# Optimization experiments

Measured on AMD Instinct MI355X. Metric: run time of the kernel, lower is better.

Reference implementation:

```python
import jax, jax.numpy as jnp
import numpy as np

K = 16  # top-k patches kept (module default)

def setup_inputs() -> dict:
    key = jax.random.key(0)
    ks = jax.random.split(key, 5)
    N, D, A, H = 100000, 1024, 128, 256
    x = jax.random.normal(ks[0], (N, D), dtype=jnp.float32)
    Wa1 = jax.random.normal(ks[1], (D, A), dtype=jnp.float32) * (1.0 / np.sqrt(D))
    ba1 = jnp.zeros((A,), dtype=jnp.float32)
    Wa2 = jax.random.normal(ks[2], (A, 1), dtype=jnp.float32) * (1.0 / np.sqrt(A))
    ba2 = jnp.zeros((1,), dtype=jnp.float32)
    Wc1 = jax.random.normal(ks[3], (D, H), dtype=jnp.float32) * (1.0 / np.sqrt(D))
    bc1 = jnp.zeros((H,), dtype=jnp.float32)
    Wc2 = jax.random.normal(ks[4], (H, 1), dtype=jnp.float32) * (1.0 / np.sqrt(H))
    bc2 = jnp.zeros((1,), dtype=jnp.float32)
    return {"x": x, "Wa1": Wa1, "ba1": ba1, "Wa2": Wa2, "ba2": ba2,
            "Wc1": Wc1, "bc1": bc1, "Wc2": Wc2, "bc2": bc2}

def reference(x, Wa1, ba1, Wa2, ba2, Wc1, bc1, Wc2, bc2):
    # attention logits: Linear -> tanh -> Linear, shape [N]
    scores = (jnp.tanh(x @ Wa1 + ba1) @ Wa2 + ba2)[:, 0]
    # top-k selection over patch dim (k < N here)
    top_vals, top_idx = jax.lax.top_k(scores, K)       # [K], [K]
    x_k = x[top_idx]                                    # [K, D] gather
    attn_w = jax.nn.softmax(top_vals)                   # renormalise over k
    slide_embedding = attn_w @ x_k                      # [D] weighted sum
    # classifier MLP (dropout is identity in eval)
    h = jax.nn.relu(slide_embedding @ Wc1 + bc1)
    logit = (h @ Wc2 + bc2)[0]
    # scatter attention weights back into full-length vector
    full_weights = jnp.zeros(x.shape[0], dtype=x.dtype).at[top_idx].set(attn_w)
    return logit, slide_embedding, full_weights, top_idx
```

## Files before the change

### kernel.cpp

```cpp
#include <hip/hip_runtime.h>
#include <cstddef>
#include <cstdint>

#define N_PATCH 100000
#define D_IN    1024
#define A_DIM   128
#define H_DIM   256
#define KTOP    16

#define OUT_LOGIT 0
#define OUT_EMB   1
#define OUT_FW    (1 + D_IN)
#define OUT_TOPI  (OUT_FW + N_PATCH)

#define WS_SCORES 0
#define WS_CANDV  (N_PATCH)
#define WS_CANDI  (N_PATCH + 4096)
#define WS_EMB    (N_PATCH + 2 * 4096)
#define WS_HPART  (WS_EMB + D_IN)
#define WS_WPK    (WS_HPART + 16 * H_DIM)

#define NB2A  256
#define CHUNK 391

typedef __attribute__((ext_vector_type(8))) short bf8_t;
typedef __attribute__((ext_vector_type(4))) float f4_t;

__global__ __launch_bounds__(256) void k_prepack(
    const float* __restrict__ Wa1, uint4* __restrict__ wpk)
{
    int t = blockIdx.x * 256 + threadIdx.x;
    int lane = t & 63;
    int part = (t >> 6) & 1;
    int nt   = (t >> 7) & 7;
    int ks   = t >> 10;
    int n  = nt * 16 + (lane & 15);
    int k0 = ks * 32 + ((lane >> 4) * 8);
    union { ushort u[8]; uint4 v; } o;
    #pragma unroll
    for (int j = 0; j < 8; ++j) {
        float w = Wa1[(size_t)(k0 + j) * A_DIM + n];
        uint b = __float_as_uint(w);
        if (part == 0) {
            o.u[j] = (ushort)(b >> 16);
        } else {
            float hf = __uint_as_float(b & 0xffff0000u);
            o.u[j] = (ushort)(__float_as_uint(w - hf) >> 16);
        }
    }
    wpk[t] = o.v;
}

__device__ __forceinline__ void split8(const float4& a, const float4& b,
                                       bf8_t& hi, bf8_t& lo)
{
    union { float f[8]; uint u[8]; float4 v4[2]; } X;
    X.v4[0] = a; X.v4[1] = b;
    union { uint u[4]; bf8_t v; } H, L;
    #pragma unroll
    for (int j = 0; j < 4; ++j) {
        uint x0 = X.u[2 * j], x1 = X.u[2 * j + 1];
        H.u[j] = __builtin_amdgcn_perm(x1, x0, 0x07060302);
        float l0 = X.f[2 * j]     - __uint_as_float(x0 & 0xffff0000u);
        float l1 = X.f[2 * j + 1] - __uint_as_float(x1 & 0xffff0000u);
        L.u[j] = __builtin_amdgcn_perm(__float_as_uint(l1), __float_as_uint(l0), 0x07060302);
    }
    hi = H.v; lo = L.v;
}

#define MFMA_BF16 __builtin_amdgcn_mfma_f32_16x16x32_bf16

#define BAR_LDS() do {                                          \
    asm volatile("s_waitcnt lgkmcnt(0)" ::: "memory");          \
    __builtin_amdgcn_s_barrier();                               \
    asm volatile("" ::: "memory");                              \
} while (0)

#define SCORE_STEP(KS, CUR) do {                                               \
    bf8_t ahi0, alo0, ahi1, alo1;                                              \
    split8(A##CUR[0], A##CUR[1], ahi0, alo0);                                  \
    split8(A##CUR[2], A##CUR[3], ahi1, alo1);                                  \
    if ((KS) < 31) {                                                           \
        _Pragma("unroll")                                                      \
        for (int i = 0; i < 4; ++i) sB[(CUR) ^ 1][tid + i * 256] = bpre[i];    \
    }                                                                          \
    {                                                                          \
        const int kact = (s0 + (KS) + 2) & 31;    \
        _Pragma("unroll")                                                      \
        for (int i = 0; i < 4; ++i) bpre[i] = wpk[kact * 1024 + tid + i * 256];\
        A##CUR[0] = *(const float4*)(pa0 + kact * 32);                         \
        A##CUR[1] = *(const float4*)(pa0 + kact * 32 + 4);                     \
        A##CUR[2] = *(const float4*)(pa1 + kact * 32);                         \
        A##CUR[3] = *(const float4*)(pa1 + kact * 32 + 4);                     \
    }                                                                          \
    const bf8_t* sBf = (const bf8_t*)sB[CUR];                                  \
    _Pragma("unroll")                                                          \
    for (int nt = 0; nt < 8; nt += 2) {                                        \
        bf8_t bh0 = sBf[(nt * 2 + 0) * 64 + ln];                               \
        bf8_t bl0 = sBf[(nt * 2 + 1) * 64 + ln];                               \
        bf8_t bh1 = sBf[(nt * 2 + 2) * 64 + ln];                               \
        bf8_t bl1 = sBf[(nt * 2 + 3) * 64 + ln];                               \
        acc[0][nt]     = MFMA_BF16(ahi0, bh0, acc[0][nt],     0, 0, 0);        \
        acc[1][nt]     = MFMA_BF16(ahi1, bh0, acc[1][nt],     0, 0, 0);        \
        acc[0][nt + 1] = MFMA_BF16(ahi0, bh1, acc[0][nt + 1], 0, 0, 0);        \
        acc[1][nt + 1] = MFMA_BF16(ahi1, bh1, acc[1][nt + 1], 0, 0, 0);        \
        acc[0][nt]     = MFMA_BF16(alo0, bh0, acc[0][nt],     0, 0, 0);        \
        acc[1][nt]     = MFMA_BF16(alo1, bh0, acc[1][nt],     0, 0, 0);        \
        acc[0][nt + 1] = MFMA_BF16(alo0, bh1, acc[0][nt + 1], 0, 0, 0);        \
        acc[1][nt + 1] = MFMA_BF16(alo1, bh1, acc[1][nt + 1], 0, 0, 0);        \
        acc[0][nt]     = MFMA_BF16(ahi0, bl0, acc[0][nt],     0, 0, 0);        \
        acc[1][nt]     = MFMA_BF16(ahi1, bl0, acc[1][nt],     0, 0, 0);        \
        acc[0][nt + 1] = MFMA_BF16(ahi0, bl1, acc[0][nt + 1], 0, 0, 0);        \
        acc[1][nt + 1] = MFMA_BF16(ahi1, bl1, acc[1][nt + 1], 0, 0, 0);        \
    }                                                                          \
    BAR_LDS();                                                                 \
} while (0)

__global__ __launch_bounds__(256) void k_scores(
    const float* __restrict__ x, const uint4* __restrict__ wpk,
    const float* __restrict__ ba1, const float* __restrict__ Wa2,
    const float* __restrict__ ba2, float* __restrict__ scores)
{
    __shared__ uint4 sB[2][1024];

    const int tid = threadIdx.x;
    const int ln  = tid & 63;
    const int q   = ln >> 4;
    const int c   = ln & 15;
    const int wv  = tid >> 6;
    const int row0 = blockIdx.x * 128 + wv * 32;
    const int s0   = blockIdx.x & 31;

    const int r0 = min(row0 + c,      N_PATCH - 1);
    const int r1 = min(row0 + 16 + c, N_PATCH - 1);
    const float* pa0 = x + (size_t)r0 * D_IN + q * 8;
    const float* pa1 = x + (size_t)r1 * D_IN + q * 8;

    f4_t acc[2][8];
    #pragma unroll
    for (int rt = 0; rt < 2; ++rt)
        #pragma unroll
        for (int nt = 0; nt < 8; ++nt)
            acc[rt][nt] = (f4_t){0.f, 0.f, 0.f, 0.f};

    uint4 bpre[4];
    {
        uint4 b0[4];
        #pragma unroll
        for (int i = 0; i < 4; ++i) b0[i] = wpk[s0 * 1024 + tid + i * 256];
        #pragma unroll
        for (int i = 0; i < 4; ++i) sB[0][tid + i * 256] = b0[i];
    }
    {
        const int k1 = (s0 + 1) & 31;
        #pragma unroll
        for (int i = 0; i < 4; ++i) bpre[i] = wpk[k1 * 1024 + tid + i * 256];
    }

    float4 A0[4], A1[4];
    {
        const int ka = s0;
        const int kb = (s0 + 1) & 31;
        A0[0] = *(const float4*)(pa0 + ka * 32);
        A0[1] = *(const float4*)(pa0 + ka * 32 + 4);
        A0[2] = *(const float4*)(pa1 + ka * 32);
        A0[3] = *(const float4*)(pa1 + ka * 32 + 4);
        A1[0] = *(const float4*)(pa0 + kb * 32);
        A1[1] = *(const float4*)(pa0 + kb * 32 + 4);
        A1[2] = *(const float4*)(pa1 + kb * 32);
        A1[3] = *(const float4*)(pa1 + kb * 32 + 4);
    }

    BAR_LDS();

    for (int ks = 0; ks < 32; ks += 2) {
        SCORE_STEP(ks,     0);
        SCORE_STEP(ks + 1, 1);
    }

    float b1v[8], w2v[8];
    #pragma unroll
    for (int nt = 0; nt < 8; ++nt) {
        b1v[nt] = ba1[nt * 16 + c];
        w2v[nt] = Wa2[nt * 16 + c];
    }
    const float b2 = ba2[0];

    #pragma unroll
    for (int rt = 0; rt < 2; ++rt)
        #pragma unroll
        for (int reg = 0; reg < 4; ++reg) {
            float p = 0.f;
            #pragma unroll
            for (int nt = 0; nt < 8; ++nt)
                p += tanhf(acc[rt][nt][reg] + b1v[nt]) * w2v[nt];
            #pragma unroll
            for (int off = 1; off < 16; off <<= 1)
                p += __shfl_xor(p, off, 64);
            if (c == 0) {
                int row = row0 + rt * 16 + q * 4 + reg;
                if (row < N_PATCH) scores[row] = p + b2;
            }
        }
}

__global__ __launch_bounds__(256) void k_topk_local(
    const float* __restrict__ scores, float* __restrict__ candv,
    int* __restrict__ candi, float* __restrict__ out_fw)
{
    __shared__ float sv[512];
    __shared__ float rv[256];
    __shared__ int   rs[256];
    const int tid  = threadIdx.x;
    const int base = blockIdx.x * CHUNK;

    for (int i = tid; i < 512; i += 256) {
        int g = base + i;
        sv[i] = (i < CHUNK && g < N_PATCH) ? scores[g] : -1e30f;
    }
    for (int i = tid; i < CHUNK; i += 256) {
        int g = base + i;
        if (g < N_PATCH) out_fw[g] = 0.f;
    }
    __syncthreads();

    for (int r = 0; r < KTOP; ++r) {
        float v1 = sv[tid], v2 = sv[tid + 256];
        float bv; int bs;
        if (v2 > v1) { bv = v2; bs = tid + 256; } else { bv = v1; bs = tid; }
        rv[tid] = bv; rs[tid] = bs;
        __syncthreads();
        for (int off = 128; off > 0; off >>= 1) {
            if (tid < off) {
                float ov = rv[tid + off]; int os = rs[tid + off];
                if (ov > rv[tid] || (ov == rv[tid] && os < rs[tid])) {
                    rv[tid] = ov; rs[tid] = os;
                }
            }
            __syncthreads();
        }
        if (tid == 0) {
            int s = rs[0];
            candv[blockIdx.x * KTOP + r] = rv[0];
            candi[blockIdx.x * KTOP + r] = base + s;
            sv[s] = -1e30f;
        }
        __syncthreads();
    }
}

__global__ __launch_bounds__(256) void k_finalize(
    const float* __restrict__ candv, const int* __restrict__ candi,
    const float* __restrict__ x, float* __restrict__ out,
    float* __restrict__ emb)
{
    __shared__ float cv[4096];
    __shared__ int   ci[4096];
    __shared__ float rv[256];
    __shared__ int   rgx[256];
    __shared__ int   rsl[256];
    __shared__ float topv[KTOP];
    __shared__ int   topi[KTOP];
    __shared__ float attn[KTOP];
    const int tid = threadIdx.x;

    for (int i = tid; i < 4096; i += 256) { cv[i] = candv[i]; ci[i] = candi[i]; }
    __syncthreads();

    for (int r = 0; r < KTOP; ++r) {
        float bv = -1e38f; int bg = 0x7fffffff; int bs = tid * 16;
        #pragma unroll
        for (int i = 0; i < 16; ++i) {
            int s = tid * 16 + i;
            float v = cv[s]; int g = ci[s];
            if (v > bv || (v == bv && g < bg)) { bv = v; bg = g; bs = s; }
        }
        rv[tid] = bv; rgx[tid] = bg; rsl[tid] = bs;
        __syncthreads();
        for (int off = 128; off > 0; off >>= 1) {
            if (tid < off) {
                if (rv[tid + off] > rv[tid] ||
                    (rv[tid + off] == rv[tid] && rgx[tid + off] < rgx[tid])) {
                    rv[tid] = rv[tid + off]; rgx[tid] = rgx[tid + off]; rsl[tid] = rsl[tid + off];
                }
            }
            __syncthreads();
        }
        if (tid == 0) {
            topv[r] = rv[0]; topi[r] = rgx[0]; cv[rsl[0]] = -1e30f;
        }
        __syncthreads();
    }

    if (tid == 0) {
        float mx = topv[0];
        float s = 0.f;
        for (int k2 = 0; k2 < KTOP; ++k2) {
            float e = expf(topv[k2] - mx);
            attn[k2] = e; s += e;
        }
        float inv = 1.f / s;
        for (int k2 = 0; k2 < KTOP; ++k2) attn[k2] *= inv;
    }
    __syncthreads();

    if (tid < KTOP) {
        out[OUT_TOPI + tid] = (float)topi[tid];
        out[OUT_FW + topi[tid]] = attn[tid];
    }

    float4 e = {0.f, 0.f, 0.f, 0.f};
    #pragma unroll
    for (int k2 = 0; k2 < KTOP; ++k2) {
        const float a = attn[k2];
        const float4 xv = *(const float4*)(x + (size_t)topi[k2] * D_IN + tid * 4);
        e.x = fmaf(a, xv.x, e.x);
        e.y = fmaf(a, xv.y, e.y);
        e.z = fmaf(a, xv.z, e.z);
        e.w = fmaf(a, xv.w, e.w);
    }
    out[OUT_EMB + tid * 4 + 0] = e.x;
    out[OUT_EMB + tid * 4 + 1] = e.y;
    out[OUT_EMB + tid * 4 + 2] = e.z;
    out[OUT_EMB + tid * 4 + 3] = e.w;
    *(float4*)(emb + tid * 4) = e;
}

__global__ __launch_bounds__(256) void k_mlp1(
    const float* __restrict__ emb, const float* __restrict__ Wc1,
    float* __restrict__ hpart)
{
    __shared__ float se[64];
    const int b = blockIdx.x, tid = threadIdx.x;
    if (tid < 64) se[tid] = emb[b * 64 + tid];
    __syncthreads();
    float p = 0.f;
    #pragma unroll 8
    for (int d = 0; d < 64; ++d)
        p = fmaf(se[d], Wc1[(size_t)(b * 64 + d) * H_DIM + tid], p);
    hpart[b * H_DIM + tid] = p;
}

__global__ __launch_bounds__(256) void k_logit(
    const float* __restrict__ hpart, const float* __restrict__ bc1,
    const float* __restrict__ Wc2, const float* __restrict__ bc2,
    float* __restrict__ out)
{
    __shared__ float red[256];
    const int tid = threadIdx.x;
    float h = bc1[tid];
    #pragma unroll
    for (int i = 0; i < 16; ++i) h += hpart[i * H_DIM + tid];
    h = fmaxf(h, 0.f) * Wc2[tid];
    red[tid] = h;
    __syncthreads();
    for (int off = 128; off > 0; off >>= 1) {
        if (tid < off) red[tid] += red[tid + off];
        __syncthreads();
    }
    if (tid == 0) out[OUT_LOGIT] = red[0] + bc2[0];
}

extern "C" void kernel_launch(void* const* d_in, const int* in_sizes, int n_in,
                              void* d_out, int out_size, void* d_ws, size_t ws_size,
                              hipStream_t stream)
{
    const float* x   = (const float*)d_in[0];
    const float* Wa1 = (const float*)d_in[1];
    const float* ba1 = (const float*)d_in[2];
    const float* Wa2 = (const float*)d_in[3];
    const float* ba2 = (const float*)d_in[4];
    const float* Wc1 = (const float*)d_in[5];
    const float* bc1 = (const float*)d_in[6];
    const float* Wc2 = (const float*)d_in[7];
    const float* bc2 = (const float*)d_in[8];
    float* out = (float*)d_out;
    float* ws  = (float*)d_ws;

    float* scores = ws + WS_SCORES;
    float* candv  = ws + WS_CANDV;
    int*   candi  = (int*)(ws + WS_CANDI);
    float* emb    = ws + WS_EMB;
    float* hpart  = ws + WS_HPART;
    uint4* wpk    = (uint4*)(ws + WS_WPK);

    dim3 blk(256);
    k_prepack<<<128, blk, 0, stream>>>(Wa1, wpk);
    k_scores<<<(N_PATCH + 127) / 128, blk, 0, stream>>>(x, wpk, ba1, Wa2, ba2, scores);
    k_topk_local<<<NB2A, blk, 0, stream>>>(scores, candv, candi, out + OUT_FW);
    k_finalize<<<1, blk, 0, stream>>>(candv, candi, x, out, emb);
    k_mlp1<<<16, blk, 0, stream>>>(emb, Wc1, hpart);
    k_logit<<<1, blk, 0, stream>>>(hpart, bc1, Wc2, bc2, out);
}
```

Measured before the change: 718.3 us.

## Score in single bf16 MFMA pass, then rescore top candidates exactly in fp32

The score GEMM drops the hi/lo bf16 split (three MFMAs per tile) and uses a single round-to-nearest bf16 product. Weight prepacking halves and the A conversion uses the hardware packed bf16 convert. To keep the selection and softmax accurate, the finalize kernel recomputes exact fp32 scores for the 16 selected rows, re-sorts them and builds attention from those values. The risk is that bf16 error changes which rows enter the top-16 candidate set. The single-block fp32 rescore also adds serial work to finalize.

Result: slower. 830.0 us (+15.5%).

```diff
diff --git a/kernel.cpp b/kernel.cpp
--- a/kernel.cpp
+++ b/kernel.cpp
@@ -31,41 +31,27 @@
 {
     int t = blockIdx.x * 256 + threadIdx.x;
     int lane = t & 63;
-    int part = (t >> 6) & 1;
-    int nt   = (t >> 7) & 7;
-    int ks   = t >> 10;
+    int nt   = (t >> 6) & 7;
+    int ks   = t >> 9;
     int n  = nt * 16 + (lane & 15);
     int k0 = ks * 32 + ((lane >> 4) * 8);
     union { ushort u[8]; uint4 v; } o;
     #pragma unroll
     for (int j = 0; j < 8; ++j) {
-        float w = Wa1[(size_t)(k0 + j) * A_DIM + n];
-        uint b = __float_as_uint(w);
-        if (part == 0) {
-            o.u[j] = (ushort)(b >> 16);
-        } else {
-            float hf = __uint_as_float(b & 0xffff0000u);
-            o.u[j] = (ushort)(__float_as_uint(w - hf) >> 16);
-        }
+        uint b = __float_as_uint(Wa1[(size_t)(k0 + j) * A_DIM + n]);
+        o.u[j] = (ushort)((b + 0x7fffu + ((b >> 16) & 1u)) >> 16);
     }
     wpk[t] = o.v;
 }
 
-__device__ __forceinline__ void split8(const float4& a, const float4& b,
-                                       bf8_t& hi, bf8_t& lo)
-{
-    union { float f[8]; uint u[8]; float4 v4[2]; } X;
-    X.v4[0] = a; X.v4[1] = b;
-    union { uint u[4]; bf8_t v; } H, L;
-    #pragma unroll
-    for (int j = 0; j < 4; ++j) {
-        uint x0 = X.u[2 * j], x1 = X.u[2 * j + 1];
-        H.u[j] = __builtin_amdgcn_perm(x1, x0, 0x07060302);
-        float l0 = X.f[2 * j]     - __uint_as_float(x0 & 0xffff0000u);
-        float l1 = X.f[2 * j + 1] - __uint_as_float(x1 & 0xffff0000u);
-        L.u[j] = __builtin_amdgcn_perm(__float_as_uint(l1), __float_as_uint(l0), 0x07060302);
-    }
-    hi = H.v; lo = L.v;
+__device__ __forceinline__ void cvt8(const float4& a, const float4& b, bf8_t& out)
+{
+    union { uint u[4]; bf8_t v; } O;
+    asm("v_cvt_pk_bf16_f32 %0, %1, %2" : "=v"(O.u[0]) : "v"(a.x), "v"(a.y));
+    asm("v_cvt_pk_bf16_f32 %0, %1, %2" : "=v"(O.u[1]) : "v"(a.z), "v"(a.w));
+    asm("v_cvt_pk_bf16_f32 %0, %1, %2" : "=v"(O.u[2]) : "v"(b.x), "v"(b.y));
+    asm("v_cvt_pk_bf16_f32 %0, %1, %2" : "=v"(O.u[3]) : "v"(b.z), "v"(b.w));
+    out = O.v;
 }
 
 #define MFMA_BF16 __builtin_amdgcn_mfma_f32_16x16x32_bf16
@@ -76,44 +62,35 @@
     asm volatile("" ::: "memory");                              \
 } while (0)
 
-#define SCORE_STEP(KS, CUR) do {                                               \
-    bf8_t ahi0, alo0, ahi1, alo1;                                              \
-    split8(A##CUR[0], A##CUR[1], ahi0, alo0);                                  \
-    split8(A##CUR[2], A##CUR[3], ahi1, alo1);                                  \
-    if ((KS) < 31) {                                                           \
+#define SCORE_STEP(IT, PAR, CUR) do {                                          \
+    bf8_t ah0, ah1;                                                            \
+    cvt8(A##CUR[0], A##CUR[1], ah0);                                           \
+    cvt8(A##CUR[2], A##CUR[3], ah1);                                           \
+    if ((PAR) == 0) {                                                          \
         _Pragma("unroll")                                                      \
-        for (int i = 0; i < 4; ++i) sB[(CUR) ^ 1][tid + i * 256] = bpre[i];    \
+        for (int i = 0; i < 4; ++i) sB[bufp ^ 1][tid + i * 256] = bpre[i];     \
+        const int vtp = (t0 + (IT) + 2) & 15;                                  \
+        _Pragma("unroll")                                                      \
+        for (int i = 0; i < 4; ++i) bpre[i] = wpk[vtp * 1024 + tid + i * 256]; \
     }                                                                          \
     {                                                                          \
-        const int kact = (s0 + (KS) + 2) & 31;    \
-        _Pragma("unroll")                                                      \
-        for (int i = 0; i < 4; ++i) bpre[i] = wpk[kact * 1024 + tid + i * 256];\
-        A##CUR[0] = *(const float4*)(pa0 + kact * 32);                         \
-        A##CUR[1] = *(const float4*)(pa0 + kact * 32 + 4);                     \
-        A##CUR[2] = *(const float4*)(pa1 + kact * 32);                         \
-        A##CUR[3] = *(const float4*)(pa1 + kact * 32 + 4);                     \
+        const int kg2 = (((t0 + (IT) + 1) & 15) * 2 + (PAR)) * 32;             \
+        A##CUR[0] = *(const float4*)(pa0 + kg2);                               \
+        A##CUR[1] = *(const float4*)(pa0 + kg2 + 4);                           \
+        A##CUR[2] = *(const float4*)(pa1 + kg2);                               \
+        A##CUR[3] = *(const float4*)(pa1 + kg2 + 4);                           \
     }                                                                          \
-    const bf8_t* sBf = (const bf8_t*)sB[CUR];                                  \
+    const bf8_t* sBf = (const bf8_t*)sB[bufp] + (PAR) * 512;                   \
     _Pragma("unroll")                                                          \
     for (int nt = 0; nt < 8; nt += 2) {                                        \
-        bf8_t bh0 = sBf[(nt * 2 + 0) * 64 + ln];                               \
-        bf8_t bl0 = sBf[(nt * 2 + 1) * 64 + ln];                               \
-        bf8_t bh1 = sBf[(nt * 2 + 2) * 64 + ln];                               \
-        bf8_t bl1 = sBf[(nt * 2 + 3) * 64 + ln];                               \
-        acc[0][nt]     = MFMA_BF16(ahi0, bh0, acc[0][nt],     0, 0, 0);        \
-        acc[1][nt]     = MFMA_BF16(ahi1, bh0, acc[1][nt],     0, 0, 0);        \
-        acc[0][nt + 1] = MFMA_BF16(ahi0, bh1, acc[0][nt + 1], 0, 0, 0);        \
-        acc[1][nt + 1] = MFMA_BF16(ahi1, bh1, acc[1][nt + 1], 0, 0, 0);        \
-        acc[0][nt]     = MFMA_BF16(alo0, bh0, acc[0][nt],     0, 0, 0);        \
-        acc[1][nt]     = MFMA_BF16(alo1, bh0, acc[1][nt],     0, 0, 0);        \
-        acc[0][nt + 1] = MFMA_BF16(alo0, bh1, acc[0][nt + 1], 0, 0, 0);        \
-        acc[1][nt + 1] = MFMA_BF16(alo1, bh1, acc[1][nt + 1], 0, 0, 0);        \
-        acc[0][nt]     = MFMA_BF16(ahi0, bl0, acc[0][nt],     0, 0, 0);        \
-        acc[1][nt]     = MFMA_BF16(ahi1, bl0, acc[1][nt],     0, 0, 0);        \
-        acc[0][nt + 1] = MFMA_BF16(ahi0, bl1, acc[0][nt + 1], 0, 0, 0);        \
-        acc[1][nt + 1] = MFMA_BF16(ahi1, bl1, acc[1][nt + 1], 0, 0, 0);        \
+        bf8_t b0 = sBf[nt * 64 + ln];                                          \
+        bf8_t b1 = sBf[(nt + 1) * 64 + ln];                                    \
+        acc[0][nt]     = MFMA_BF16(ah0, b0, acc[0][nt],     0, 0, 0);          \
+        acc[1][nt]     = MFMA_BF16(ah1, b0, acc[1][nt],     0, 0, 0);          \
+        acc[0][nt + 1] = MFMA_BF16(ah0, b1, acc[0][nt + 1], 0, 0, 0);          \
+        acc[1][nt + 1] = MFMA_BF16(ah1, b1, acc[1][nt + 1], 0, 0, 0);          \
     }                                                                          \
-    BAR_LDS();                                                                 \
+    if (PAR) BAR_LDS();                                                        \
 } while (0)
 
 __global__ __launch_bounds__(256) void k_scores(
@@ -129,7 +106,7 @@
     const int c   = ln & 15;
     const int wv  = tid >> 6;
     const int row0 = blockIdx.x * 128 + wv * 32;
-    const int s0   = blockIdx.x & 31;
+    const int t0   = blockIdx.x & 15;
 
     const int r0 = min(row0 + c,      N_PATCH - 1);
     const int r1 = min(row0 + 16 + c, N_PATCH - 1);
@@ -147,35 +124,36 @@
     {
         uint4 b0[4];
         #pragma unroll
-        for (int i = 0; i < 4; ++i) b0[i] = wpk[s0 * 1024 + tid + i * 256];
+        for (int i = 0; i < 4; ++i) b0[i] = wpk[t0 * 1024 + tid + i * 256];
         #pragma unroll
         for (int i = 0; i < 4; ++i) sB[0][tid + i * 256] = b0[i];
     }
     {
-        const int k1 = (s0 + 1) & 31;
-        #pragma unroll
-        for (int i = 0; i < 4; ++i) bpre[i] = wpk[k1 * 1024 + tid + i * 256];
+        const int t1 = (t0 + 1) & 15;
+        #pragma unroll
+        for (int i = 0; i < 4; ++i) bpre[i] = wpk[t1 * 1024 + tid + i * 256];
     }
 
     float4 A0[4], A1[4];
     {
-        const int ka = s0;
-        const int kb = (s0 + 1) & 31;
-        A0[0] = *(const float4*)(pa0 + ka * 32);
-        A0[1] = *(const float4*)(pa0 + ka * 32 + 4);
-        A0[2] = *(const float4*)(pa1 + ka * 32);
-        A0[3] = *(const float4*)(pa1 + ka * 32 + 4);
-        A1[0] = *(const float4*)(pa0 + kb * 32);
-        A1[1] = *(const float4*)(pa0 + kb * 32 + 4);
-        A1[2] = *(const float4*)(pa1 + kb * 32);
-        A1[3] = *(const float4*)(pa1 + kb * 32 + 4);
+        const int ka = (t0 * 2) * 32;
+        const int kb = (t0 * 2 + 1) * 32;
+        A0[0] = *(const float4*)(pa0 + ka);
+        A0[1] = *(const float4*)(pa0 + ka + 4);
+        A0[2] = *(const float4*)(pa1 + ka);
+        A0[3] = *(const float4*)(pa1 + ka + 4);
+        A1[0] = *(const float4*)(pa0 + kb);
+        A1[1] = *(const float4*)(pa0 + kb + 4);
+        A1[2] = *(const float4*)(pa1 + kb);
+        A1[3] = *(const float4*)(pa1 + kb + 4);
     }
 
     BAR_LDS();
 
-    for (int ks = 0; ks < 32; ks += 2) {
-        SCORE_STEP(ks,     0);
-        SCORE_STEP(ks + 1, 1);
+    for (int it = 0; it < 16; ++it) {
+        const int bufp = it & 1;
+        SCORE_STEP(it, 0, 0);
+        SCORE_STEP(it, 1, 1);
     }
 
     float b1v[8], w2v[8];
@@ -251,7 +229,9 @@
 
 __global__ __launch_bounds__(256) void k_finalize(
     const float* __restrict__ candv, const int* __restrict__ candi,
-    const float* __restrict__ x, float* __restrict__ out,
+    const float* __restrict__ x, const float* __restrict__ Wa1,
+    const float* __restrict__ ba1, const float* __restrict__ Wa2,
+    const float* __restrict__ ba2, float* __restrict__ out,
     float* __restrict__ emb)
 {
     __shared__ float cv[4096];
@@ -259,9 +239,12 @@
     __shared__ float rv[256];
     __shared__ int   rgx[256];
     __shared__ int   rsl[256];
-    __shared__ float topv[KTOP];
     __shared__ int   topi[KTOP];
+    __shared__ float sxs[KTOP][D_IN] __attribute__((aligned(16)));
+    __shared__ float sred[KTOP][128];
+    __shared__ float exv[KTOP];
     __shared__ float attn[KTOP];
+    __shared__ int   order[KTOP];
     const int tid = threadIdx.x;
 
     for (int i = tid; i < 4096; i += 256) { cv[i] = candv[i]; ci[i] = candi[i]; }
@@ -287,33 +270,74 @@
             __syncthreads();
         }
         if (tid == 0) {
-            topv[r] = rv[0]; topi[r] = rgx[0]; cv[rsl[0]] = -1e30f;
+            topi[r] = rgx[0]; cv[rsl[0]] = -1e30f;
         }
         __syncthreads();
     }
 
+    for (int r = 0; r < KTOP; ++r)
+        for (int d = tid; d < D_IN; d += 256)
+            sxs[r][d] = x[(size_t)topi[r] * D_IN + d];
+    __syncthreads();
+
+    {
+        const int g = tid >> 7, n = tid & 127;
+        float ac[8];
+        #pragma unroll
+        for (int rr = 0; rr < 8; ++rr) ac[rr] = 0.f;
+        #pragma unroll 4
+        for (int d = 0; d < D_IN; ++d) {
+            const float w = Wa1[(size_t)d * A_DIM + n];
+            #pragma unroll
+            for (int rr = 0; rr < 8; ++rr)
+                ac[rr] = fmaf(sxs[g * 8 + rr][d], w, ac[rr]);
+        }
+        const float bn = ba1[n], wn = Wa2[n];
+        #pragma unroll
+        for (int rr = 0; rr < 8; ++rr)
+            sred[g * 8 + rr][n] = tanhf(ac[rr] + bn) * wn;
+    }
+    __syncthreads();
+    if (tid < KTOP) {
+        float s = ba2[0];
+        for (int n = 0; n < 128; ++n) s += sred[tid][n];
+        exv[tid] = s;
+    }
+    __syncthreads();
+
     if (tid == 0) {
-        float mx = topv[0];
-        float s = 0.f;
+        #pragma unroll
+        for (int k2 = 0; k2 < KTOP; ++k2) order[k2] = k2;
+        for (int a2 = 1; a2 < KTOP; ++a2)
+            for (int b2 = a2; b2 > 0; --b2) {
+                int i1 = order[b2 - 1], i2 = order[b2];
+                bool sw = (exv[i2] > exv[i1]) ||
+                          (exv[i2] == exv[i1] && topi[i2] < topi[i1]);
+                if (sw) { order[b2 - 1] = i2; order[b2] = i1; } else break;
+            }
+        float mx = exv[order[0]];
+        float ssum = 0.f;
         for (int k2 = 0; k2 < KTOP; ++k2) {
-            float e = expf(topv[k2] - mx);
-            attn[k2] = e; s += e;
-        }
-        float inv = 1.f / s;
+            float e = expf(exv[order[k2]] - mx);
+            attn[k2] = e; ssum += e;
+        }
+        float inv = 1.f / ssum;
         for (int k2 = 0; k2 < KTOP; ++k2) attn[k2] *= inv;
     }
     __syncthreads();
 
     if (tid < KTOP) {
-        out[OUT_TOPI + tid] = (float)topi[tid];
-        out[OUT_FW + topi[tid]] = attn[tid];
+        int src = order[tid];
+        out[OUT_TOPI + tid] = (float)topi[src];
+        out[OUT_FW + topi[src]] = attn[tid];
     }
 
     float4 e = {0.f, 0.f, 0.f, 0.f};
     #pragma unroll
     for (int k2 = 0; k2 < KTOP; ++k2) {
+        const int src = order[k2];
         const float a = attn[k2];
-        const float4 xv = *(const float4*)(x + (size_t)topi[k2] * D_IN + tid * 4);
+        const float4 xv = *(const float4*)(&sxs[src][tid * 4]);
         e.x = fmaf(a, xv.x, e.x);
         e.y = fmaf(a, xv.y, e.y);
         e.z = fmaf(a, xv.z, e.z);
@@ -385,10 +409,10 @@
     uint4* wpk    = (uint4*)(ws + WS_WPK);
 
     dim3 blk(256);
-    k_prepack<<<128, blk, 0, stream>>>(Wa1, wpk);
+    k_prepack<<<64, blk, 0, stream>>>(Wa1, wpk);
     k_scores<<<(N_PATCH + 127) / 128, blk, 0, stream>>>(x, wpk, ba1, Wa2, ba2, scores);
     k_topk_local<<<NB2A, blk, 0, stream>>>(scores, candv, candi, out + OUT_FW);
-    k_finalize<<<1, blk, 0, stream>>>(candv, candi, x, out, emb);
+    k_finalize<<<1, blk, 0, stream>>>(candv, candi, x, Wa1, ba1, Wa2, ba2, out, emb);
     k_mlp1<<<16, blk, 0, stream>>>(emb, Wc1, hpart);
     k_logit<<<1, blk, 0, stream>>>(hpart, bc1, Wc2, bc2, out);
 }
```
